# Optimization experiments

Measured on AMD Instinct MI355X. Metric: run time of the kernel, lower is better.

The kernel has to match this reference:

```python
import jax, jax.numpy as jnp
import numpy as np

B, L, G, N, K, E = 64, 512, 128, 32, 8, 65536
NTOK, D_TOK, H_DIR, NTL_INP, NHID, NREL = 10000, 64, 64, 32, 16, 16


def _bn(x, gamma, beta, eps=1e-5):
    # training-mode BatchNorm1d over axis 0; x: (n, C)
    mu = x.mean(0)
    var = x.var(0)
    return gamma * (x - mu) / jnp.sqrt(var + eps) + beta


def _lstm(x, w_ih, w_hh, b_ih, b_hh):
    # x: (B, T, D); torch gate order i, f, g, o
    nb = x.shape[0]
    H = w_hh.shape[1]
    def step(carry, xt):
        h, c = carry
        g = xt @ w_ih.T + b_ih + h @ w_hh.T + b_hh
        i, f, gg, o = jnp.split(g, 4, axis=-1)
        c = jax.nn.sigmoid(f) * c + jax.nn.sigmoid(i) * jnp.tanh(gg)
        h = jax.nn.sigmoid(o) * jnp.tanh(c)
        return (h, c), h
    init = (jnp.zeros((nb, H), x.dtype), jnp.zeros((nb, H), x.dtype))
    _, hs = jax.lax.scan(step, init, jnp.swapaxes(x, 0, 1))
    return jnp.swapaxes(hs, 0, 1)


def setup_inputs() -> dict:
    key = jax.random.key(0)
    ks = jax.random.split(key, 24)
    inp = {}
    inp['seq'] = jax.random.randint(ks[0], (B, L), 0, NTOK)
    inp['pos2grp'] = jax.random.randint(ks[1], (B, L), 0, G)
    inp['idx'] = jax.random.randint(ks[2], (B, N, K), 0, L)
    inp['u'] = jax.random.randint(ks[3], (E,), 0, B * N)
    inp['v'] = jax.random.randint(ks[4], (E,), 0, B * N)
    # parameters
    s = 1.0 / np.sqrt(H_DIR)
    inp['tok_emb'] = jax.random.normal(ks[5], (NTOK, D_TOK), jnp.float32)
    for tag, k0 in (('f', 6), ('b', 10)):
        inp[f'w_ih_{tag}'] = s * jax.random.normal(ks[k0], (4 * H_DIR, D_TOK), jnp.float32)
        inp[f'w_hh_{tag}'] = s * jax.random.normal(ks[k0 + 1], (4 * H_DIR, H_DIR), jnp.float32)
        inp[f'b_ih_{tag}'] = s * jax.random.normal(ks[k0 + 2], (4 * H_DIR,), jnp.float32)
        inp[f'b_hh_{tag}'] = s * jax.random.normal(ks[k0 + 3], (4 * H_DIR,), jnp.float32)
    inp['w_src'] = (1.0 / np.sqrt(2 * H_DIR)) * jax.random.normal(ks[14], (NTL_INP, 2 * H_DIR), jnp.float32)
    inp['b_src'] = jnp.zeros((NTL_INP,), jnp.float32)
    inp['w_dst'] = (1.0 / np.sqrt(2 * H_DIR)) * jax.random.normal(ks[15], (NTL_INP, 2 * H_DIR), jnp.float32)
    inp['b_dst'] = jnp.zeros((NTL_INP,), jnp.float32)
    inp['g_src'] = jnp.ones((NTL_INP,), jnp.float32)
    inp['be_src'] = jnp.zeros((NTL_INP,), jnp.float32)
    inp['g_dst'] = jnp.ones((NTL_INP,), jnp.float32)
    inp['be_dst'] = jnp.zeros((NTL_INP,), jnp.float32)
    inp['ntl_w'] = 0.001 * jax.random.normal(ks[16], (NREL, NHID, NTL_INP, NTL_INP), jnp.float32)
    inp['ntl_v'] = 0.001 * jax.random.normal(ks[17], (NREL, NHID, 2 * NTL_INP), jnp.float32)
    inp['ntl_b'] = jnp.zeros((NREL, NHID, 1), jnp.float32)
    inp['ntl_u'] = 0.001 * jax.random.normal(ks[18], (NREL, 1, NHID), jnp.float32)
    inp['ntl_g'] = jnp.ones((NREL * NHID,), jnp.float32)
    inp['ntl_be'] = jnp.zeros((NREL * NHID,), jnp.float32)
    return inp


def reference(seq, pos2grp, idx, u, v, tok_emb,
              w_ih_f, w_hh_f, b_ih_f, b_hh_f,
              w_ih_b, w_hh_b, b_ih_b, b_hh_b,
              w_src, b_src, w_dst, b_dst,
              g_src, be_src, g_dst, be_dst,
              ntl_w, ntl_v, ntl_b, ntl_u, ntl_g, ntl_be):
    # token embed + scatter-sum tokens -> groups
    x_tok = tok_emb[seq]                                   # (B, L, D)
    gid = (pos2grp + jnp.arange(B)[:, None] * G).reshape(-1)
    x_grp = jax.ops.segment_sum(x_tok.reshape(B * L, -1), gid,
                                num_segments=B * G).reshape(B, G, -1)
    # bidirectional LSTM over groups
    hf = _lstm(x_grp, w_ih_f, w_hh_f, b_ih_f, b_hh_f)
    hb = jnp.flip(_lstm(jnp.flip(x_grp, 1), w_ih_b, w_hh_b, b_ih_b, b_hh_b), 1)
    h_grp = jnp.concatenate([hf, hb], -1)                  # (B, G, 2H)
    # hierarchical gather + sum: node <- sum over K token positions' groups
    b_idx = jnp.arange(B)[:, None, None]
    g_idx = pos2grp[b_idx, idx]                            # (B, N, K)
    h = h_grp[b_idx, g_idx].sum(2).reshape(B * N, -1)      # (B*N, 2H)
    # edge endpoint projections + batchnorm
    hs = _bn(h[u] @ w_src.T + b_src, g_src, be_src)        # (E, ninp)
    ht = _bn(h[v] @ w_dst.T + b_dst, g_dst, be_dst)
    # Neural Tensor Layer
    linear = jnp.einsum('rhd,nd->rhn', ntl_v, jnp.concatenate([hs, ht], 1))
    bil = jnp.stack([
        jnp.einsum('nhj,nj->hn', jnp.einsum('ni,hij->nhj', hs, ntl_w[r]), ht)
        for r in range(NREL)], 0)                          # (R, H, E)
    z = bil + linear + ntl_b
    mu = z.mean(-1, keepdims=True)
    var = z.var(-1, keepdims=True)
    zn = ntl_g.reshape(NREL, NHID, 1) * (z - mu) / jnp.sqrt(var + 1e-5) \
         + ntl_be.reshape(NREL, NHID, 1)
    t = jnp.tanh(zn)
    logit = jnp.einsum('rh,rhn->nr', ntl_u[:, 0, :], t)    # (E, R)
    return logit
```

## Files before the change

### kernel.cpp

```cpp
#include <hip/hip_runtime.h>
#include <hip/hip_bf16.h>
#include <cstdint>

constexpr int B_   = 64;
constexpr int L_   = 512;
constexpr int G_   = 128;
constexpr int E_   = 65536;
constexpr int RH   = 256;
constexpr int M_   = 2048;
constexpr int JA   = 33;
constexpr int COLS = RH * JA;
constexpr int STRD = 36;

#define DEV static __device__ __forceinline__

DEV float sigm(float x) { return 1.f / (1.f + __expf(-x)); }
DEV float tanh_fast(float x) {
    x = fminf(15.f, fmaxf(-15.f, x));
    float e = __expf(2.f * x);
    return (e - 1.f) / (e + 1.f);
}
DEV int rfl(int x) { return __builtin_amdgcn_readfirstlane(x); }
DEV float rdlane(float x, int lane) {
    return __int_as_float(__builtin_amdgcn_readlane(__float_as_int(x), lane));
}

__global__ __launch_bounds__(256) void k_eh(const int* __restrict__ seq,
                                            const int* __restrict__ p2g,
                                            const float* __restrict__ emb,
                                            const int* __restrict__ u,
                                            const int* __restrict__ v,
                                            float* __restrict__ xg,
                                            int* __restrict__ cu, int* __restrict__ cv) {
    int blk = blockIdx.x;
    int t   = threadIdx.x;
    if (blk >= 64) {
        int n = (blk - 64) * 256 + t;
        atomicAdd(&cu[u[n]], 1);
        atomicAdd(&cv[v[n]], 1);
        return;
    }
    __shared__ float xgl[G_ * 64];
    for (int i = t; i < G_ * 64; i += 256) xgl[i] = 0.f;
    __syncthreads();
    int b = blk;
    int d = t & 63, part = t >> 6;
#pragma unroll 8
    for (int l = part; l < L_; l += 4) {
        int s = seq[b * L_ + l];
        int g = p2g[b * L_ + l];
        atomicAdd(&xgl[g * 64 + d], emb[s * 64 + d]);
    }
    __syncthreads();
    for (int i = t; i < G_ * 64; i += 256) xg[(size_t)b * G_ * 64 + i] = xgl[i];
}

__global__ __launch_bounds__(256) void k_pre(const float* __restrict__ xg,
                                             const float* __restrict__ wihf,
                                             const float* __restrict__ bihf,
                                             const float* __restrict__ bhhf,
                                             const float* __restrict__ wihb,
                                             const float* __restrict__ bihb,
                                             const float* __restrict__ bhhb,
                                             float* __restrict__ pre,
                                             const int* __restrict__ cu,
                                             int* __restrict__ ustart,
                                             int* __restrict__ ucursor) {
    int blk = blockIdx.x;
    int t   = threadIdx.x;
    if (blk == 512) {
        __shared__ int ps[256];
        int base = t * 8, run = 0;
        int c[8], loc[8];
#pragma unroll
        for (int i = 0; i < 8; i++) c[i] = cu[base + i];
#pragma unroll
        for (int i = 0; i < 8; i++) { loc[i] = run; run += c[i]; }
        ps[t] = run;
        __syncthreads();
        for (int off = 1; off < 256; off <<= 1) {
            int a = (t >= off) ? ps[t - off] : 0;
            __syncthreads();
            ps[t] += a;
            __syncthreads();
        }
        int ex = ps[t] - run;
#pragma unroll
        for (int i = 0; i < 8; i++) { ustart[base + i] = ex + loc[i]; ucursor[base + i] = ex + loc[i]; }
        if (t == 255) ustart[2048] = E_;
        return;
    }
    int dir = blk >> 8;
    const float* wih = dir ? wihb : wihf;
    float bias = dir ? (bihb[t] + bhhb[t]) : (bihf[t] + bhhf[t]);
    int r0 = (blk & 255) * 32;

    float4 wv[16];
#pragma unroll
    for (int c = 0; c < 16; c++) wv[c] = ((const float4*)(wih + t * 64))[c];

#pragma unroll 2
    for (int ml = 0; ml < 32; ml++) {
        const float* xr = xg + (size_t)(r0 + ml) * 64;
        float acc = bias;
#pragma unroll
        for (int c = 0; c < 16; c++) {
            float x0 = xr[4 * c], x1 = xr[4 * c + 1], x2 = xr[4 * c + 2], x3 = xr[4 * c + 3];
            acc += x0 * wv[c].x + x1 * wv[c].y + x2 * wv[c].z + x3 * wv[c].w;
        }
        pre[((size_t)dir * 8192 + r0 + ml) * 256 + t] = acc;
    }
}

__global__ __launch_bounds__(256, 1) void k_lstm(const float* __restrict__ pre,
                                                 const float* __restrict__ whh_f,
                                                 const float* __restrict__ whh_b,
                                                 float* __restrict__ hgrp,
                                                 const int* __restrict__ u,
                                                 const int* __restrict__ v,
                                                 int* __restrict__ ucursor,
                                                 int2* __restrict__ eonv) {
    int blk = blockIdx.x;
    int t   = threadIdx.x;
    if (blk >= 128) {
        int n = (blk - 128) * 256 + t;
        int pos = atomicAdd(&ucursor[u[n]], 1);
        eonv[pos] = make_int2(n, v[n]);
        return;
    }
    __shared__ __align__(16) float plds[64][256];
    __shared__ __align__(16) float hist[64][64];
    __shared__ float gl[2][256];
    int dir = blk >> 6;
    int b   = blk & 63;
    const float* whh = dir ? whh_b : whh_f;
    const float* src = pre + ((size_t)dir * 8192 + (size_t)b * G_) * 256;
    int e = t & 63;
    int q = t >> 6;

    float4 wv[16];
#pragma unroll
    for (int c = 0; c < 16; c++) wv[c] = ((const float4*)(whh + (size_t)t * 64))[c];

    float h = 0.f, creg = 0.f;

    for (int half = 0; half < 2; half++) {
        {
            int base = (dir ^ half) ? 64 : 0;
            const float4* s4 = (const float4*)(src + (size_t)base * 256);
            float4* d4 = (float4*)&plds[0][0];
#pragma unroll
            for (int i = 0; i < 16; i++) d4[i * 256 + t] = s4[i * 256 + t];
        }
        __syncthreads();
        for (int kk = 0; kk < 64; kk++) {
            int k = half * 64 + kk;
            int srow = dir ? (63 - kk) : kk;
            float p = plds[srow][t];
            float a0 = p, a1 = 0.f, a2 = 0.f, a3 = 0.f;
#pragma unroll
            for (int c = 0; c < 16; c++) {
                float f0 = rdlane(h, 4 * c + 0);
                float f1 = rdlane(h, 4 * c + 1);
                float f2 = rdlane(h, 4 * c + 2);
                float f3 = rdlane(h, 4 * c + 3);
                a0 += wv[c].x * f0;
                a1 += wv[c].y * f1;
                a2 += wv[c].z * f2;
                a3 += wv[c].w * f3;
            }
            float g = (a0 + a1) + (a2 + a3);
            gl[k & 1][t] = (q == 2) ? tanh_fast(g) : sigm(g);
            __syncthreads();
            float ai = gl[k & 1][e];
            float af = gl[k & 1][64 + e];
            float ag = gl[k & 1][128 + e];
            float ao = gl[k & 1][192 + e];
            creg = af * creg + ai * ag;
            h = ao * tanh_fast(creg);
            if (q == 0) hist[srow][e] = h;
        }
        __syncthreads();
        int sbase = (dir ? (1 - half) : half) * 64;
#pragma unroll
        for (int i = 0; i < 16; i++) {
            int row = q * 16 + i;
            int s = sbase + row;
            hgrp[((size_t)(b * G_ + s)) * 128 + dir * 64 + e] = hist[row][e];
        }
    }
}

__global__ __launch_bounds__(256) void k_gp(const int* __restrict__ idx,
                                            const int* __restrict__ p2g,
                                            const float* __restrict__ hgrp,
                                            const int* __restrict__ cu,
                                            const int* __restrict__ cv,
                                            const float* __restrict__ wsrc,
                                            const float* __restrict__ bsrc,
                                            const float* __restrict__ wdst,
                                            const float* __restrict__ bdst,
                                            float* __restrict__ Ps, float* __restrict__ Pd,
                                            float* __restrict__ bn_raw) {
    __shared__ __align__(16) float hsl[8][128];
    __shared__ float red[256];
    int m0 = blockIdx.x * 8;
    int t  = threadIdx.x;
    int d = t & 127, mh = t >> 7;
#pragma unroll
    for (int rep = 0; rep < 4; rep++) {
        int ml = rep * 2 + mh;
        int m  = m0 + ml;
        int b  = m >> 5;
        float acc = 0.f;
#pragma unroll
        for (int k = 0; k < 8; k++) {
            int l = idx[m * 8 + k];
            int g = p2g[b * L_ + l];
            acc += hgrp[((size_t)b * G_ + g) * 128 + d];
        }
        hsl[ml][d] = acc;
    }
    __syncthreads();
    int ml = t >> 5, o = t & 31;
    int m  = m0 + ml;
    const float4* hp = (const float4*)&hsl[ml][0];
    float cw_u = (float)cu[m], cw_v = (float)cv[m];
#pragma unroll 1
    for (int side = 0; side < 2; side++) {
        const float* W = side ? wdst : wsrc;
        float4 wr[32];
#pragma unroll
        for (int c = 0; c < 32; c++) wr[c] = ((const float4*)(W + (size_t)o * 128))[c];
        float acc = side ? bdst[o] : bsrc[o];
#pragma unroll
        for (int c = 0; c < 32; c++) {
            float4 h4 = hp[c];
            acc += h4.x * wr[c].x + h4.y * wr[c].y + h4.z * wr[c].z + h4.w * wr[c].w;
        }
        (side ? Pd : Ps)[(size_t)m * 32 + o] = acc;
        float cw = side ? cw_v : cw_u;
        red[t] = cw * acc;
        __syncthreads();
        if (t < 32) {
            float s = 0.f;
#pragma unroll
            for (int i = 0; i < 8; i++) s += red[i * 32 + t];
            atomicAdd(&bn_raw[side * 64 + t], s);
        }
        __syncthreads();
        red[t] = cw * acc * acc;
        __syncthreads();
        if (t < 32) {
            float s = 0.f;
#pragma unroll
            for (int i = 0; i < 8; i++) s += red[i * 32 + t];
            atomicAdd(&bn_raw[side * 64 + 32 + t], s);
        }
        __syncthreads();
    }
}

__global__ __launch_bounds__(256) void k_prep(const float* __restrict__ Ps,
                                              const float* __restrict__ Pd,
                                              const float* __restrict__ bn_raw,
                                              const float* __restrict__ gs,
                                              const float* __restrict__ bes,
                                              const float* __restrict__ gd,
                                              const float* __restrict__ bed,
                                              const float* __restrict__ ntlw,
                                              const float* __restrict__ ntlv,
                                              const float* __restrict__ ntlb,
                                              float* __restrict__ hsaug,
                                              float* __restrict__ htaug,
                                              float* __restrict__ waug) {
    int blk = blockIdx.x;
    int t   = threadIdx.x;
    constexpr float invE = 1.f / (float)E_;
    if (blk < 576) {
        int gid = blk * 256 + t;
        int m = gid / (2 * STRD), s2 = gid % (2 * STRD);
        if (s2 < STRD) {
            int i = s2;
            float val = 0.f;
            if (i < 32) {
                float mu  = bn_raw[i] * invE;
                float isd = rsqrtf(bn_raw[32 + i] * invE - mu * mu + 1e-5f);
                val = gs[i] * (Ps[(size_t)m * 32 + i] - mu) * isd + bes[i];
            } else if (i == 32) val = 1.f;
            hsaug[(size_t)m * STRD + i] = val;
        } else {
            int j = s2 - STRD;
            float val = 0.f;
            if (j < 32) {
                float mu  = bn_raw[64 + j] * invE;
                float isd = rsqrtf(bn_raw[96 + j] * invE - mu * mu + 1e-5f);
                val = gd[j] * (Pd[(size_t)m * 32 + j] - mu) * isd + bed[j];
            } else if (j == 32) val = 1.f;
            htaug[(size_t)m * STRD + j] = val;
        }
        return;
    }
    int gid = (blk - 576) * 256 + t;
    int i   = gid / COLS;
    int rem = gid - i * COLS;
    int rh  = rem / JA;
    int j   = rem - rh * JA;
    float val;
    if (i < 32) val = (j < 32) ? ntlw[((size_t)rh * 32 + i) * 32 + j] : ntlv[rh * 64 + i];
    else        val = (j < 32) ? ntlv[rh * 64 + 32 + j] : ntlb[rh];
    waug[(size_t)i * COLS + j * 256 + rh] = val;
}

__global__ __launch_bounds__(256) void k_agemm(const float* __restrict__ hsaug,
                                               const float* __restrict__ waug,
                                               __hip_bfloat16* __restrict__ A) {
    int mt = blockIdx.x;
    int j  = blockIdx.y;
    int t  = threadIdx.x;
    float w[JA];
#pragma unroll
    for (int i = 0; i < JA; i++) w[i] = waug[(size_t)i * COLS + j * 256 + t];

#pragma unroll 2
    for (int ml = 0; ml < 32; ml++) {
        const float* hr = hsaug + (size_t)(mt * 32 + ml) * STRD;
        float a0 = 0.f, a1 = 0.f;
#pragma unroll
        for (int i = 0; i < 32; i += 2) {
            a0 += hr[i] * w[i];
            a1 += hr[i + 1] * w[i + 1];
        }
        float acc = a0 + a1 + hr[32] * w[32];
        A[(size_t)(mt * 32 + ml) * COLS + j * 256 + t] = __float2bfloat16(acc);
    }
}

DEV void load_ht(float* d, const float* __restrict__ htaug, int vv) {
    const float* hp = htaug + (size_t)vv * STRD;
#pragma unroll
    for (int j = 0; j < JA; j++) d[j] = hp[j];
}
DEV void edge_compute(const float* av, const float* ht, int n, int t,
                      __hip_bfloat16* __restrict__ z, float& s1, float& s2) {
    float a0 = 0.f, a1 = 0.f;
#pragma unroll
    for (int j = 0; j < 32; j += 2) {
        a0 += av[j] * ht[j];
        a1 += av[j + 1] * ht[j + 1];
    }
    float acc = a0 + a1 + av[32] * ht[32];
    z[(size_t)n * 256 + t] = __float2bfloat16(acc);
    s1 += acc; s2 += acc * acc;
}

__global__ __launch_bounds__(256) void k_z(const __hip_bfloat16* __restrict__ A,
                                           const float* __restrict__ htaug,
                                           const int* __restrict__ ustart,
                                           const int2* __restrict__ eonv,
                                           __hip_bfloat16* __restrict__ z,
                                           float* __restrict__ zsum,
                                           float* __restrict__ zsq) {
    int t  = threadIdx.x;
    int uu = blockIdx.x;
    float s1 = 0.f, s2 = 0.f;
    float av[JA];
#pragma unroll
    for (int j = 0; j < JA; j++)
        av[j] = __bfloat162float(A[(size_t)uu * COLS + j * 256 + t]);
    int e0 = ustart[uu], e1 = ustart[uu + 1];
    if (e0 < e1) {
        int e = e0;
        int2 q0 = eonv[e];
        int n0 = rfl(q0.x), v0 = rfl(q0.y);
        float ht0[JA]; load_ht(ht0, htaug, v0);
        int n1 = 0; float ht1[JA];
        while (true) {
            if (e + 1 < e1) {
                int2 q = eonv[e + 1];
                n1 = rfl(q.x); int v1 = rfl(q.y);
                load_ht(ht1, htaug, v1);
            }
            edge_compute(av, ht0, n0, t, z, s1, s2);
            if (++e >= e1) break;
            if (e + 1 < e1) {
                int2 q = eonv[e + 1];
                n0 = rfl(q.x); int v0b = rfl(q.y);
                load_ht(ht0, htaug, v0b);
            }
            edge_compute(av, ht1, n1, t, z, s1, s2);
            if (++e >= e1) break;
        }
    }
    atomicAdd(&zsum[t], s1);
    atomicAdd(&zsq[t], s2);
}

__global__ __launch_bounds__(256) void k_logit(const __hip_bfloat16* __restrict__ z,
                                               const float* __restrict__ zsum,
                                               const float* __restrict__ zsq,
                                               const float* __restrict__ ntlu,
                                               const float* __restrict__ ntlg,
                                               const float* __restrict__ ntlbe,
                                               float* __restrict__ out) {
    int t  = threadIdx.x;
    int n0 = blockIdx.x * 16;
    float mu  = zsum[t] / (float)E_;
    float var = zsq[t] / (float)E_ - mu * mu;
    float isd = rsqrtf(var + 1e-5f);
    float g   = ntlg[t],  be  = ntlbe[t];
    float uw  = ntlu[t];
    float zv[16];
#pragma unroll
    for (int nl = 0; nl < 16; nl++)
        zv[nl] = __bfloat162float(z[(size_t)(n0 + nl) * 256 + t]);
#pragma unroll 1
    for (int nl = 0; nl < 16; nl++) {
        float zn  = g * (zv[nl] - mu) * isd + be;
        float val = uw * tanh_fast(zn);
        val += __shfl_xor(val, 1);
        val += __shfl_xor(val, 2);
        val += __shfl_xor(val, 4);
        val += __shfl_xor(val, 8);
        if ((t & 15) == 0) out[(size_t)(n0 + nl) * 16 + (t >> 4)] = val;
    }
}

extern "C" void kernel_launch(void* const* d_in, const int* in_sizes, int n_in,
                              void* d_out, int out_size, void* d_ws, size_t ws_size,
                              hipStream_t stream) {
    const int*   seq   = (const int*)d_in[0];
    const int*   p2g   = (const int*)d_in[1];
    const int*   idx   = (const int*)d_in[2];
    const int*   u     = (const int*)d_in[3];
    const int*   v     = (const int*)d_in[4];
    const float* emb   = (const float*)d_in[5];
    const float* wihf  = (const float*)d_in[6];
    const float* whhf  = (const float*)d_in[7];
    const float* bihf  = (const float*)d_in[8];
    const float* bhhf  = (const float*)d_in[9];
    const float* wihb  = (const float*)d_in[10];
    const float* whhb  = (const float*)d_in[11];
    const float* bihb  = (const float*)d_in[12];
    const float* bhhb  = (const float*)d_in[13];
    const float* wsrc  = (const float*)d_in[14];
    const float* bsrc  = (const float*)d_in[15];
    const float* wdst  = (const float*)d_in[16];
    const float* bdst  = (const float*)d_in[17];
    const float* gs    = (const float*)d_in[18];
    const float* bes   = (const float*)d_in[19];
    const float* gd    = (const float*)d_in[20];
    const float* bed   = (const float*)d_in[21];
    const float* ntlw  = (const float*)d_in[22];
    const float* ntlv  = (const float*)d_in[23];
    const float* ntlb  = (const float*)d_in[24];
    const float* ntlu  = (const float*)d_in[25];
    const float* ntlg  = (const float*)d_in[26];
    const float* ntlbe = (const float*)d_in[27];
    float* out = (float*)d_out;

    char* ws = (char*)d_ws;
    size_t off = 0;
    auto take = [&](size_t bytes) -> char* {
        char* p = ws + off;
        off = (off + bytes + 255) & ~(size_t)255;
        return p;
    };
    int*   cnt_u  = (int*)  take(2048 * 4);
    int*   cnt_v  = (int*)  take(2048 * 4);
    float* zsum   = (float*)take(256 * 4);
    float* zsq    = (float*)take(256 * 4);
    float* bn_raw = (float*)take(128 * 4);
    size_t zero_bytes = off;
    float* x_grp   = (float*)take((size_t)B_ * G_ * 64 * 4);
    int*   ucursor = (int*)  take(2048 * 4);
    int*   ustart  = (int*)  take(2049 * 4);
    int2*  eonv    = (int2*) take((size_t)E_ * 8);
    float* pre     = (float*)take((size_t)2 * 8192 * 256 * 4);
    float* hgrp    = (float*)take((size_t)B_ * G_ * 128 * 4);
    float* Psrc    = (float*)take((size_t)M_ * 32 * 4);
    float* Pdst    = (float*)take((size_t)M_ * 32 * 4);
    float* hsaug   = (float*)take((size_t)M_ * STRD * 4);
    float* htaug   = (float*)take((size_t)M_ * STRD * 4);
    float* waug    = (float*)take((size_t)JA * COLS * 4);
    __hip_bfloat16* Abuf = (__hip_bfloat16*)take((size_t)M_ * COLS * 2);
    __hip_bfloat16* zbuf = (__hip_bfloat16*)take((size_t)E_ * 256 * 2);
    (void)ws_size; (void)in_sizes; (void)n_in; (void)out_size;

    hipMemsetAsync(d_ws, 0, zero_bytes, stream);

    k_eh<<<320, 256, 0, stream>>>(seq, p2g, emb, u, v, x_grp, cnt_u, cnt_v);
    k_pre<<<513, 256, 0, stream>>>(x_grp, wihf, bihf, bhhf, wihb, bihb, bhhb, pre,
                                   cnt_u, ustart, ucursor);
    k_lstm<<<384, 256, 0, stream>>>(pre, whhf, whhb, hgrp, u, v, ucursor, eonv);
    k_gp<<<M_ / 8, 256, 0, stream>>>(idx, p2g, hgrp, cnt_u, cnt_v,
                                     wsrc, bsrc, wdst, bdst, Psrc, Pdst, bn_raw);
    k_prep<<<576 + 1089, 256, 0, stream>>>(Psrc, Pdst, bn_raw, gs, bes, gd, bed,
                                           ntlw, ntlv, ntlb, hsaug, htaug, waug);
    k_agemm<<<dim3(64, JA), 256, 0, stream>>>(hsaug, waug, Abuf);
    k_z<<<M_, 256, 0, stream>>>(Abuf, htaug, ustart, eonv, zbuf, zsum, zsq);
    k_logit<<<E_ / 16, 256, 0, stream>>>(zbuf, zsum, zsq, ntlu, ntlg, ntlbe, out);
}
```

Measured before the change: 417.5 us.

## Switch NTL bilinear stage to packed fp16 dot2 with transposed GEMM inputs

Converts the per-edge bilinear contraction from scalar bf16→fp32 FMAs to packed fp16 pairs using the fdot2 instruction. The A matrix is stored as fp16 pairs, with the bias column kept in fp32, and ht is packed to fp16. The weight-augmentation transform moves into the first kernel's spare blocks so it runs off the critical path. hsaug is transposed so the A-GEMM accumulates 32 rows per thread with broadcast loads, and z is now stored as fp16. This is meant to halve the ALU work and bandwidth in the hot edge loop, at the cost of fp16 range and precision risk.

After: 411.8 us. About the same (-1.4%).

```diff
diff --git a/kernel.cpp b/kernel.cpp
--- a/kernel.cpp
+++ b/kernel.cpp
@@ -1,5 +1,6 @@
 #include <hip/hip_runtime.h>
 #include <hip/hip_bf16.h>
+#include <hip/hip_fp16.h>
 #include <cstdint>
 
 constexpr int B_   = 64;
@@ -10,7 +11,8 @@
 constexpr int M_   = 2048;
 constexpr int JA   = 33;
 constexpr int COLS = RH * JA;
-constexpr int STRD = 36;
+
+typedef _Float16 v2h __attribute__((ext_vector_type(2)));
 
 #define DEV static __device__ __forceinline__
 
@@ -21,19 +23,33 @@
     return (e - 1.f) / (e + 1.f);
 }
 DEV int rfl(int x) { return __builtin_amdgcn_readfirstlane(x); }
-DEV float rdlane(float x, int lane) {
-    return __int_as_float(__builtin_amdgcn_readlane(__float_as_int(x), lane));
-}
+DEV v2h bch(unsigned int x) { union { unsigned int u; v2h h; } c; c.u = x; return c.h; }
 
 __global__ __launch_bounds__(256) void k_eh(const int* __restrict__ seq,
                                             const int* __restrict__ p2g,
                                             const float* __restrict__ emb,
                                             const int* __restrict__ u,
                                             const int* __restrict__ v,
+                                            const float* __restrict__ ntlw,
+                                            const float* __restrict__ ntlv,
+                                            const float* __restrict__ ntlb,
                                             float* __restrict__ xg,
-                                            int* __restrict__ cu, int* __restrict__ cv) {
+                                            int* __restrict__ cu, int* __restrict__ cv,
+                                            float* __restrict__ waug) {
     int blk = blockIdx.x;
     int t   = threadIdx.x;
+    if (blk >= 320) {
+        int gid = (blk - 320) * 256 + t;
+        int i   = gid / COLS;
+        int rem = gid - i * COLS;
+        int j   = rem >> 8;
+        int rh  = rem & 255;
+        float val;
+        if (i < 32) val = (j < 32) ? ntlw[((size_t)rh * 32 + i) * 32 + j] : ntlv[rh * 64 + i];
+        else        val = (j < 32) ? ntlv[rh * 64 + 32 + j] : ntlb[rh];
+        waug[gid] = val;
+        return;
+    }
     if (blk >= 64) {
         int n = (blk - 64) * 256 + t;
         atomicAdd(&cu[u[n]], 1);
@@ -160,10 +176,10 @@
             float a0 = p, a1 = 0.f, a2 = 0.f, a3 = 0.f;
 #pragma unroll
             for (int c = 0; c < 16; c++) {
-                float f0 = rdlane(h, 4 * c + 0);
-                float f1 = rdlane(h, 4 * c + 1);
-                float f2 = rdlane(h, 4 * c + 2);
-                float f3 = rdlane(h, 4 * c + 3);
+                float f0 = __int_as_float(__builtin_amdgcn_readlane(__float_as_int(h), 4 * c + 0));
+                float f1 = __int_as_float(__builtin_amdgcn_readlane(__float_as_int(h), 4 * c + 1));
+                float f2 = __int_as_float(__builtin_amdgcn_readlane(__float_as_int(h), 4 * c + 2));
+                float f3 = __int_as_float(__builtin_amdgcn_readlane(__float_as_int(h), 4 * c + 3));
                 a0 += wv[c].x * f0;
                 a1 += wv[c].y * f1;
                 a2 += wv[c].z * f2;
@@ -268,127 +284,142 @@
                                               const float* __restrict__ bes,
                                               const float* __restrict__ gd,
                                               const float* __restrict__ bed,
-                                              const float* __restrict__ ntlw,
-                                              const float* __restrict__ ntlv,
-                                              const float* __restrict__ ntlb,
-                                              float* __restrict__ hsaug,
-                                              float* __restrict__ htaug,
-                                              float* __restrict__ waug) {
+                                              float* __restrict__ hsaugT,
+                                              v2h* __restrict__ htp) {
     int blk = blockIdx.x;
     int t   = threadIdx.x;
     constexpr float invE = 1.f / (float)E_;
-    if (blk < 576) {
+    if (blk < 264) {
         int gid = blk * 256 + t;
-        int m = gid / (2 * STRD), s2 = gid % (2 * STRD);
-        if (s2 < STRD) {
-            int i = s2;
-            float val = 0.f;
-            if (i < 32) {
-                float mu  = bn_raw[i] * invE;
-                float isd = rsqrtf(bn_raw[32 + i] * invE - mu * mu + 1e-5f);
-                val = gs[i] * (Ps[(size_t)m * 32 + i] - mu) * isd + bes[i];
-            } else if (i == 32) val = 1.f;
-            hsaug[(size_t)m * STRD + i] = val;
-        } else {
-            int j = s2 - STRD;
-            float val = 0.f;
-            if (j < 32) {
-                float mu  = bn_raw[64 + j] * invE;
-                float isd = rsqrtf(bn_raw[96 + j] * invE - mu * mu + 1e-5f);
-                val = gd[j] * (Pd[(size_t)m * 32 + j] - mu) * isd + bed[j];
-            } else if (j == 32) val = 1.f;
-            htaug[(size_t)m * STRD + j] = val;
-        }
+        int c = gid >> 11;
+        int m = gid & 2047;
+        float val = 1.f;
+        if (c < 32) {
+            float mu  = bn_raw[c] * invE;
+            float isd = rsqrtf(bn_raw[32 + c] * invE - mu * mu + 1e-5f);
+            val = gs[c] * (Ps[(size_t)m * 32 + c] - mu) * isd + bes[c];
+        }
+        hsaugT[(size_t)c * 2048 + m] = val;
         return;
     }
-    int gid = (blk - 576) * 256 + t;
-    int i   = gid / COLS;
-    int rem = gid - i * COLS;
-    int rh  = rem / JA;
-    int j   = rem - rh * JA;
-    float val;
-    if (i < 32) val = (j < 32) ? ntlw[((size_t)rh * 32 + i) * 32 + j] : ntlv[rh * 64 + i];
-    else        val = (j < 32) ? ntlv[rh * 64 + 32 + j] : ntlb[rh];
-    waug[(size_t)i * COLS + j * 256 + rh] = val;
-}
-
-__global__ __launch_bounds__(256) void k_agemm(const float* __restrict__ hsaug,
+    int gid = (blk - 264) * 256 + t;
+    int m  = gid >> 4;
+    int jp = gid & 15;
+    int j0 = 2 * jp, j1 = 2 * jp + 1;
+    float mu0  = bn_raw[64 + j0] * invE;
+    float isd0 = rsqrtf(bn_raw[96 + j0] * invE - mu0 * mu0 + 1e-5f);
+    float mu1  = bn_raw[64 + j1] * invE;
+    float isd1 = rsqrtf(bn_raw[96 + j1] * invE - mu1 * mu1 + 1e-5f);
+    float h0 = gd[j0] * (Pd[(size_t)m * 32 + j0] - mu0) * isd0 + bed[j0];
+    float h1 = gd[j1] * (Pd[(size_t)m * 32 + j1] - mu1) * isd1 + bed[j1];
+    v2h p;
+    p.x = (_Float16)h0; p.y = (_Float16)h1;
+    htp[gid] = p;
+}
+
+__global__ __launch_bounds__(256) void k_agemm(const float* __restrict__ hsaugT,
                                                const float* __restrict__ waug,
-                                               __hip_bfloat16* __restrict__ A) {
+                                               v2h* __restrict__ Ah,
+                                               float* __restrict__ A32) {
     int mt = blockIdx.x;
-    int j  = blockIdx.y;
+    int jp = blockIdx.y;
     int t  = threadIdx.x;
-    float w[JA];
-#pragma unroll
-    for (int i = 0; i < JA; i++) w[i] = waug[(size_t)i * COLS + j * 256 + t];
-
-#pragma unroll 2
-    for (int ml = 0; ml < 32; ml++) {
-        const float* hr = hsaug + (size_t)(mt * 32 + ml) * STRD;
-        float a0 = 0.f, a1 = 0.f;
-#pragma unroll
-        for (int i = 0; i < 32; i += 2) {
-            a0 += hr[i] * w[i];
-            a1 += hr[i + 1] * w[i + 1];
-        }
-        float acc = a0 + a1 + hr[32] * w[32];
-        A[(size_t)(mt * 32 + ml) * COLS + j * 256 + t] = __float2bfloat16(acc);
-    }
-}
-
-DEV void load_ht(float* d, const float* __restrict__ htaug, int vv) {
-    const float* hp = htaug + (size_t)vv * STRD;
-#pragma unroll
-    for (int j = 0; j < JA; j++) d[j] = hp[j];
-}
-DEV void edge_compute(const float* av, const float* ht, int n, int t,
-                      __hip_bfloat16* __restrict__ z, float& s1, float& s2) {
-    float a0 = 0.f, a1 = 0.f;
-#pragma unroll
-    for (int j = 0; j < 32; j += 2) {
-        a0 += av[j] * ht[j];
-        a1 += av[j + 1] * ht[j + 1];
-    }
-    float acc = a0 + a1 + av[32] * ht[32];
-    z[(size_t)n * 256 + t] = __float2bfloat16(acc);
+    if (jp < 16) {
+        float w0[JA], w1[JA];
+#pragma unroll
+        for (int i = 0; i < JA; i++) {
+            w0[i] = waug[(size_t)i * COLS + (2 * jp) * 256 + t];
+            w1[i] = waug[(size_t)i * COLS + (2 * jp + 1) * 256 + t];
+        }
+        float acc0[32], acc1[32];
+#pragma unroll
+        for (int ml = 0; ml < 32; ml++) { acc0[ml] = 0.f; acc1[ml] = 0.f; }
+#pragma unroll 3
+        for (int i = 0; i < JA; i++) {
+            const float* hr = hsaugT + (size_t)i * 2048 + mt * 32;
+#pragma unroll
+            for (int ml = 0; ml < 32; ml++) {
+                acc0[ml] += hr[ml] * w0[i];
+                acc1[ml] += hr[ml] * w1[i];
+            }
+        }
+#pragma unroll
+        for (int ml = 0; ml < 32; ml++) {
+            v2h p;
+            p.x = (_Float16)acc0[ml]; p.y = (_Float16)acc1[ml];
+            Ah[(size_t)(mt * 32 + ml) * 4096 + jp * 256 + t] = p;
+        }
+    } else {
+        float w2[JA];
+#pragma unroll
+        for (int i = 0; i < JA; i++) w2[i] = waug[(size_t)i * COLS + 32 * 256 + t];
+        float acc[32];
+#pragma unroll
+        for (int ml = 0; ml < 32; ml++) acc[ml] = 0.f;
+#pragma unroll 3
+        for (int i = 0; i < JA; i++) {
+            const float* hr = hsaugT + (size_t)i * 2048 + mt * 32;
+#pragma unroll
+            for (int ml = 0; ml < 32; ml++) acc[ml] += hr[ml] * w2[i];
+        }
+#pragma unroll
+        for (int ml = 0; ml < 32; ml++)
+            A32[(size_t)(mt * 32 + ml) * 256 + t] = acc[ml];
+    }
+}
+
+DEV void load_htp(unsigned int* d, const unsigned int* __restrict__ htp, int vv) {
+    const unsigned int* hp = htp + vv * 16;
+#pragma unroll
+    for (int i = 0; i < 16; i++) d[i] = hp[i];
+}
+DEV void edge_fd(const unsigned int* av, const unsigned int* ht, float av32,
+                 int n, int t, _Float16* __restrict__ zh, float& s1, float& s2) {
+    float acc = av32;
+#pragma unroll
+    for (int jp = 0; jp < 16; jp++)
+        acc = __builtin_amdgcn_fdot2(bch(av[jp]), bch(ht[jp]), acc, false);
+    zh[(size_t)n * 256 + t] = (_Float16)acc;
     s1 += acc; s2 += acc * acc;
 }
 
-__global__ __launch_bounds__(256) void k_z(const __hip_bfloat16* __restrict__ A,
-                                           const float* __restrict__ htaug,
+__global__ __launch_bounds__(256) void k_z(const unsigned int* __restrict__ Ah,
+                                           const float* __restrict__ A32,
+                                           const unsigned int* __restrict__ htp,
                                            const int* __restrict__ ustart,
                                            const int2* __restrict__ eonv,
-                                           __hip_bfloat16* __restrict__ z,
+                                           _Float16* __restrict__ zh,
                                            float* __restrict__ zsum,
                                            float* __restrict__ zsq) {
     int t  = threadIdx.x;
     int uu = blockIdx.x;
     float s1 = 0.f, s2 = 0.f;
-    float av[JA];
-#pragma unroll
-    for (int j = 0; j < JA; j++)
-        av[j] = __bfloat162float(A[(size_t)uu * COLS + j * 256 + t]);
+    unsigned int av[16];
+#pragma unroll
+    for (int jp = 0; jp < 16; jp++)
+        av[jp] = Ah[(size_t)uu * 4096 + jp * 256 + t];
+    float av32 = A32[(size_t)uu * 256 + t];
     int e0 = ustart[uu], e1 = ustart[uu + 1];
     if (e0 < e1) {
         int e = e0;
         int2 q0 = eonv[e];
         int n0 = rfl(q0.x), v0 = rfl(q0.y);
-        float ht0[JA]; load_ht(ht0, htaug, v0);
-        int n1 = 0; float ht1[JA];
+        unsigned int ht0[16]; load_htp(ht0, htp, v0);
+        int n1 = 0; unsigned int ht1[16];
         while (true) {
             if (e + 1 < e1) {
                 int2 q = eonv[e + 1];
                 n1 = rfl(q.x); int v1 = rfl(q.y);
-                load_ht(ht1, htaug, v1);
+                load_htp(ht1, htp, v1);
             }
-            edge_compute(av, ht0, n0, t, z, s1, s2);
+            edge_fd(av, ht0, av32, n0, t, zh, s1, s2);
             if (++e >= e1) break;
             if (e + 1 < e1) {
                 int2 q = eonv[e + 1];
                 n0 = rfl(q.x); int v0b = rfl(q.y);
-                load_ht(ht0, htaug, v0b);
+                load_htp(ht0, htp, v0b);
             }
-            edge_compute(av, ht1, n1, t, z, s1, s2);
+            edge_fd(av, ht1, av32, n1, t, zh, s1, s2);
             if (++e >= e1) break;
         }
     }
@@ -396,7 +427,7 @@
     atomicAdd(&zsq[t], s2);
 }
 
-__global__ __launch_bounds__(256) void k_logit(const __hip_bfloat16* __restrict__ z,
+__global__ __launch_bounds__(256) void k_logit(const _Float16* __restrict__ zh,
                                                const float* __restrict__ zsum,
                                                const float* __restrict__ zsq,
                                                const float* __restrict__ ntlu,
@@ -413,7 +444,7 @@
     float zv[16];
 #pragma unroll
     for (int nl = 0; nl < 16; nl++)
-        zv[nl] = __bfloat162float(z[(size_t)(n0 + nl) * 256 + t]);
+        zv[nl] = (float)zh[(size_t)(n0 + nl) * 256 + t];
 #pragma unroll 1
     for (int nl = 0; nl < 16; nl++) {
         float zn  = g * (zv[nl] - mu) * isd + be;
@@ -480,24 +511,26 @@
     float* hgrp    = (float*)take((size_t)B_ * G_ * 128 * 4);
     float* Psrc    = (float*)take((size_t)M_ * 32 * 4);
     float* Pdst    = (float*)take((size_t)M_ * 32 * 4);
-    float* hsaug   = (float*)take((size_t)M_ * STRD * 4);
-    float* htaug   = (float*)take((size_t)M_ * STRD * 4);
+    float* hsaugT  = (float*)take((size_t)36 * 2048 * 4);
+    v2h*   htp     = (v2h*)  take((size_t)M_ * 16 * 4);
     float* waug    = (float*)take((size_t)JA * COLS * 4);
-    __hip_bfloat16* Abuf = (__hip_bfloat16*)take((size_t)M_ * COLS * 2);
-    __hip_bfloat16* zbuf = (__hip_bfloat16*)take((size_t)E_ * 256 * 2);
+    v2h*   Ah      = (v2h*)  take((size_t)M_ * 4096 * 4);
+    float* A32     = (float*)take((size_t)M_ * 256 * 4);
+    _Float16* zbuf = (_Float16*)take((size_t)E_ * 256 * 2);
     (void)ws_size; (void)in_sizes; (void)n_in; (void)out_size;
 
     hipMemsetAsync(d_ws, 0, zero_bytes, stream);
 
-    k_eh<<<320, 256, 0, stream>>>(seq, p2g, emb, u, v, x_grp, cnt_u, cnt_v);
+    k_eh<<<320 + 1089, 256, 0, stream>>>(seq, p2g, emb, u, v, ntlw, ntlv, ntlb,
+                                         x_grp, cnt_u, cnt_v, waug);
     k_pre<<<513, 256, 0, stream>>>(x_grp, wihf, bihf, bhhf, wihb, bihb, bhhb, pre,
                                    cnt_u, ustart, ucursor);
     k_lstm<<<384, 256, 0, stream>>>(pre, whhf, whhb, hgrp, u, v, ucursor, eonv);
     k_gp<<<M_ / 8, 256, 0, stream>>>(idx, p2g, hgrp, cnt_u, cnt_v,
                                      wsrc, bsrc, wdst, bdst, Psrc, Pdst, bn_raw);
-    k_prep<<<576 + 1089, 256, 0, stream>>>(Psrc, Pdst, bn_raw, gs, bes, gd, bed,
-                                           ntlw, ntlv, ntlb, hsaug, htaug, waug);
-    k_agemm<<<dim3(64, JA), 256, 0, stream>>>(hsaug, waug, Abuf);
-    k_z<<<M_, 256, 0, stream>>>(Abuf, htaug, ustart, eonv, zbuf, zsum, zsq);
+    k_prep<<<392, 256, 0, stream>>>(Psrc, Pdst, bn_raw, gs, bes, gd, bed, hsaugT, htp);
+    k_agemm<<<dim3(64, 17), 256, 0, stream>>>(hsaugT, waug, Ah, A32);
+    k_z<<<M_, 256, 0, stream>>>((const unsigned int*)Ah, A32, (const unsigned int*)htp,
+                                ustart, eonv, zbuf, zsum, zsq);
     k_logit<<<E_ / 16, 256, 0, stream>>>(zbuf, zsum, zsq, ntlu, ntlg, ntlbe, out);
 }
```
